# Optimization experiments

Hardware: AMD Instinct MI355X
Metric: run time of the kernel (lower is better)

## Reference

```python
import jax, jax.numpy as jnp
import numpy as np

H, C, PQ, PV = 12, 16, 4, 8  # heads, scalar head dim, query points, value points
EPS = 1e-8


def setup_inputs() -> dict:
    key = jax.random.key(0)
    ks = jax.random.split(key, 16)
    B, N, S, Z = 2, 512, 384, 128
    def w(k, fan_in, shape):
        return jax.random.normal(k, shape, jnp.float32) / np.sqrt(fan_in)
    return {
        's': jax.random.normal(ks[0], (B, N, S), jnp.float32),
        'z': jax.random.normal(ks[1], (B, N, N, Z), jnp.float32),
        'R': jax.random.normal(ks[2], (B, N, 3, 3), jnp.float32),
        't': jax.random.normal(ks[3], (B, N, 3), jnp.float32),
        'Wq': w(ks[4], S, (S, H * C)),
        'Wk': w(ks[5], S, (S, H * C)),
        'Wv': w(ks[6], S, (S, H * C)),
        'Wqp': w(ks[7], S, (S, H * PQ * 3)),
        'Wkp': w(ks[8], S, (S, H * PQ * 3)),
        'Wvp': w(ks[9], S, (S, H * PV * 3)),
        'Wb': w(ks[10], Z, (Z, H)),
        'head_weights': jax.random.normal(ks[11], (H,), jnp.float32) * 0.1,
        'Wout': w(ks[12], H * (C + 4 * PV + Z), (H * (C + 4 * PV + Z), S)),
    }


def reference(s, z, R, t, Wq, Wk, Wv, Wqp, Wkp, Wvp, Wb, head_weights, Wout):
    B, N, _ = s.shape
    Zc = z.shape[-1]
    # scalar q/k/v: [B,N,H,C]
    q = (s @ Wq).reshape(B, N, H, C)
    k = (s @ Wk).reshape(B, N, H, C)
    v = (s @ Wv).reshape(B, N, H, C)
    # point q/k/v in local frames, then map to global: x_g = R x + t
    def to_global(Wp, P):
        p = (s @ Wp).reshape(B, N, H, P, 3)
        return jnp.einsum('bnxy,bnhpy->bnhpx', R, p) + t[:, :, None, None, :]
    qp = to_global(Wqp, PQ)   # [B,N,H,PQ,3]
    kp = to_global(Wkp, PQ)
    vp = to_global(Wvp, PV)   # [B,N,H,PV,3]
    # pair bias [B,H,N,N]
    b = jnp.einsum('bijz,zh->bhij', z, Wb)
    # scalar attention logits
    scal = jnp.einsum('bihc,bjhc->bhij', q, k) / np.sqrt(C)
    # squared point distances via expansion (avoid [B,N,N,H,PQ,3] tensor)
    qq = jnp.sum(qp * qp, axis=(-1, -2))                    # [B,N,H]
    kk = jnp.sum(kp * kp, axis=(-1, -2))                    # [B,N,H]
    qk = jnp.einsum('bihpx,bjhpx->bhij', qp, kp)
    dist2 = qq.transpose(0, 2, 1)[:, :, :, None] + kk.transpose(0, 2, 1)[:, :, None, :] - 2.0 * qk
    gamma = jax.nn.softplus(head_weights)                   # [H]
    wC = np.sqrt(2.0 / (9.0 * PQ))
    wL = np.sqrt(1.0 / 3.0)
    logits = wL * (scal + b) - (wL * wC / 2.0) * gamma[None, :, None, None] * dist2
    a = jax.nn.softmax(logits, axis=-1)                     # [B,H,N,N]
    # scalar output
    o = jnp.einsum('bhij,bjhc->bihc', a, v).reshape(B, N, H * C)
    # point output: aggregate in global frame, then back to local: R^T (x - t)
    opt_g = jnp.einsum('bhij,bjhpx->bihpx', a, vp)
    d = opt_g - t[:, :, None, None, :]
    opt = jnp.einsum('bnyx,bnhpy->bnhpx', R, d)             # R^T d
    opt_norm = jnp.sqrt(jnp.sum(opt * opt, axis=-1) + EPS)  # [B,N,H,PV]
    # pair output
    opair = jnp.einsum('bhij,bijz->bihz', a, z).reshape(B, N, H * Zc)
    cat = jnp.concatenate([o, opt.reshape(B, N, H * PV * 3),
                           opt_norm.reshape(B, N, H * PV), opair], axis=-1)
    return cat @ Wout
```

## Files before the change

### kernel.cpp

```cpp
#include <hip/hip_runtime.h>
#include <math.h>

#define BB 2
#define NN 512
#define SDIM 384
#define ZDIM 128
#define HH 12
#define CDIM 16
#define PQ 4
#define PV 8
#define BN (BB*NN)
#define CATD 2112

#define WL  0.57735026918962576f
#define LAM 0.06804138174397717f

#define OFF_Q    0
#define OFF_QP   196608
#define OFF_QQ   344064
#define OFF_KT4  356352
#define OFF_KPT4 552960
#define OFF_KKT  700416
#define OFF_V    712704
#define OFF_VP   909312
#define OFF_CAT  7495680

__device__ __forceinline__ float dot4(float4 a, float4 b) {
    return a.x*b.x + a.y*b.y + a.z*b.z + a.w*b.w;
}
__device__ __forceinline__ void fma4(float4& a, float s, float4 b) {
    a.x += s*b.x; a.y += s*b.y; a.z += s*b.z; a.w += s*b.w;
}
__device__ __forceinline__ void add4(float4& a, float4 b) {
    a.x += b.x; a.y += b.y; a.z += b.z; a.w += b.w;
}
__device__ __forceinline__ void mul4(float4& a, float s) {
    a.x *= s; a.y *= s; a.z *= s; a.w *= s;
}

__global__ __launch_bounds__(256) void k_proj(
    const float* __restrict__ s, const float* __restrict__ Rg, const float* __restrict__ tg,
    const float* __restrict__ Wq, const float* __restrict__ Wk, const float* __restrict__ Wv,
    const float* __restrict__ Wqp, const float* __restrict__ Wkp, const float* __restrict__ Wvp,
    float* __restrict__ ws)
{
    __shared__ float4 pL4[2][144];
    __shared__ float  sqL[2][96];
    __shared__ float  Rt[2][12];
    const int t = threadIdx.x;
    const int n0 = blockIdx.x * 2;
    const int b  = n0 >> 9;
    const int nloc = n0 & 511;

    if (t < 24) {
        int rr = t / 12, c = t % 12;
        Rt[rr][c] = (c < 9) ? Rg[(n0+rr)*9 + c] : tg[(n0+rr)*3 + (c-9)];
    }
    const float* s0 = s + (size_t)n0*SDIM;
    const float* s1 = s0 + SDIM;
    __syncthreads();

    float4* Q4g  = (float4*)(ws + OFF_Q);
    float4* V4g  = (float4*)(ws + OFF_V);
    float4* KT4g = (float4*)(ws + OFF_KT4);

    for (int it = 0; it < 2; ++it) {
        int g = t + it*256;
        if (g >= 288) break;
        const float4* W4; int wc4, ld4, dst;
        if (g < 48)       { W4 = (const float4*)Wq;  wc4 = g;     ld4 = 48; dst = 0; }
        else if (g < 96)  { W4 = (const float4*)Wk;  wc4 = g-48;  ld4 = 48; dst = 1; }
        else if (g < 144) { W4 = (const float4*)Wv;  wc4 = g-96;  ld4 = 48; dst = 2; }
        else if (g < 180) { W4 = (const float4*)Wqp; wc4 = g-144; ld4 = 36; dst = 3; }
        else if (g < 216) { W4 = (const float4*)Wkp; wc4 = g-180; ld4 = 36; dst = 4; }
        else              { W4 = (const float4*)Wvp; wc4 = g-216; ld4 = 72; dst = 5; }
        float4 acc0 = {0,0,0,0}, acc1 = {0,0,0,0};
        #pragma unroll 4
        for (int r = 0; r < SDIM; ++r) {
            float4 wv = W4[r*ld4 + wc4];
            float f0 = s0[r], f1 = s1[r];
            fma4(acc0, f0, wv);
            fma4(acc1, f1, wv);
        }
        if (dst == 0) {
            Q4g[(size_t)n0*48 + wc4] = acc0;
            Q4g[(size_t)(n0+1)*48 + wc4] = acc1;
        } else if (dst == 1) {
            size_t base = ((size_t)(b*48 + wc4))*512 + nloc;
            KT4g[base] = acc0; KT4g[base+1] = acc1;
        } else if (dst == 2) {
            V4g[(size_t)n0*48 + wc4] = acc0;
            V4g[(size_t)(n0+1)*48 + wc4] = acc1;
        } else if (dst == 3) {
            pL4[0][wc4] = acc0; pL4[1][wc4] = acc1;
        } else if (dst == 4) {
            pL4[0][36+wc4] = acc0; pL4[1][36+wc4] = acc1;
        } else {
            pL4[0][72+wc4] = acc0; pL4[1][72+wc4] = acc1;
        }
    }
    __syncthreads();

    for (int task = t; task < 384; task += 256) {
        int rr = task / 192, pt = task % 192;
        const float* pl = (const float*)pL4[rr];
        int off = (pt < 48) ? pt*3 : (pt < 96 ? 144 + (pt-48)*3 : 288 + (pt-96)*3);
        float p0 = pl[off], p1 = pl[off+1], p2 = pl[off+2];
        const float* R = Rt[rr];
        float g0 = R[0]*p0 + R[1]*p1 + R[2]*p2 + R[9];
        float g1 = R[3]*p0 + R[4]*p1 + R[5]*p2 + R[10];
        float g2 = R[6]*p0 + R[7]*p1 + R[8]*p2 + R[11];
        int bn = n0 + rr, n = bn & 511;
        if (pt < 48) {
            int o = pt*3;
            float* d = ws + OFF_QP + (size_t)bn*144 + o;
            d[0] = g0; d[1] = g1; d[2] = g2;
            sqL[rr][pt] = g0*g0 + g1*g1 + g2*g2;
        } else if (pt < 96) {
            int pc = (pt-48)*3;
            float gg[3] = {g0,g1,g2};
            #pragma unroll
            for (int x = 0; x < 3; ++x) {
                int pcx = pc + x;
                ws[OFF_KPT4 + (((size_t)(b*36 + (pcx>>2)))*512 + n)*4 + (pcx&3)] = gg[x];
            }
            sqL[rr][pt] = g0*g0 + g1*g1 + g2*g2;
        } else {
            int o = (pt-96)*3;
            float* d = ws + OFF_VP + (size_t)bn*288 + o;
            d[0] = g0; d[1] = g1; d[2] = g2;
        }
    }
    __syncthreads();

    if (t < 48) {
        int rr = t / 24, u = t % 24;
        int bn = n0 + rr, n = bn & 511;
        if (u < 12) {
            float sm = sqL[rr][u*4] + sqL[rr][u*4+1] + sqL[rr][u*4+2] + sqL[rr][u*4+3];
            ws[OFF_QQ + (size_t)bn*12 + u] = sm;
        } else {
            int h = u - 12;
            float sm = sqL[rr][48+h*4] + sqL[rr][48+h*4+1] + sqL[rr][48+h*4+2] + sqL[rr][48+h*4+3];
            ws[OFF_KKT + ((size_t)(b*12 + h))*512 + n] = sm;
        }
    }
}

__global__ __launch_bounds__(512, 2) void k_attn(
    const float* __restrict__ z, const float* __restrict__ Rg, const float* __restrict__ tg,
    const float* __restrict__ hw, const float* __restrict__ Wb, float* __restrict__ ws)
{
    __shared__ __align__(16) float aL[8448];
    __shared__ float4 optgS4[72];
    __shared__ float RiL[9], tiL[3], sInv[12];

    const int t = threadIdx.x;
    const int d = blockIdx.x;
    const int xcd = d & 7, slot = d >> 3;
    const int bi = (xcd < 4) ? (xcd*128 + slot) : (512 + (xcd-4)*128 + slot);
    const int b = bi >> 9;

    if (t < 9)             RiL[t]   = Rg[bi*9 + t];
    if (t >= 9 && t < 12)  tiL[t-9] = tg[bi*3 + (t-9)];

    float gam[HH];
    #pragma unroll
    for (int h = 0; h < HH; ++h) {
        float x = hw[h];
        gam[h] = (x > 20.f) ? x : log1pf(__expf(x));
    }

    {
        const int j = t;
        float pb[HH];
        #pragma unroll
        for (int h = 0; h < HH; ++h) pb[h] = 0.f;
        const float4* zrow4 = (const float4*)z + ((size_t)bi*512 + j)*32;
        #pragma unroll 4
        for (int c4 = 0; c4 < 32; ++c4) {
            const float4 zq = zrow4[c4];
            const float* wb = Wb + c4*48;
            #pragma unroll
            for (int e = 0; e < 4; ++e) {
                const float zv = ((const float*)&zq)[e];
                const float* w = wb + e*12;
                #pragma unroll
                for (int h = 0; h < HH; ++h) pb[h] += zv * w[h];
            }
        }
        const float4* Q4u  = (const float4*)(ws + OFF_Q  + (size_t)bi*192);
        const float4* QP4u = (const float4*)(ws + OFF_QP + (size_t)bi*144);
        const float*  QQu  = ws + OFF_QQ + (size_t)bi*12;
        const float4* KT4  = (const float4*)(ws + OFF_KT4)  + (size_t)b*48*512;
        const float4* KPT4 = (const float4*)(ws + OFF_KPT4) + (size_t)b*36*512;
        const float*  KKT  = ws + OFF_KKT  + (size_t)b*12*512;
        for (int h = 0; h < HH; ++h) {
            float scal = 0.f, qk = 0.f;
            #pragma unroll
            for (int cg = 0; cg < 4; ++cg)
                scal += dot4(Q4u[h*4+cg], KT4[(h*4+cg)*512 + j]);
            #pragma unroll
            for (int pg = 0; pg < 3; ++pg)
                qk += dot4(QP4u[h*3+pg], KPT4[(h*3+pg)*512 + j]);
            float dist2 = QQu[h] + KKT[h*512 + j] - 2.f*qk;
            aL[h*516 + j] = WL*(scal*0.25f + pb[h]) - LAM*gam[h]*dist2;
        }
    }
    __syncthreads();

    {
        const int w = t >> 6, lane = t & 63;
        for (int h = w; h < HH; h += 8) {
            float* row = aL + h*516;
            float m = -1e30f;
            #pragma unroll
            for (int k = 0; k < 8; ++k) m = fmaxf(m, row[lane + 64*k]);
            #pragma unroll
            for (int off = 32; off > 0; off >>= 1) m = fmaxf(m, __shfl_xor(m, off));
            float ssum = 0.f;
            #pragma unroll
            for (int k = 0; k < 8; ++k) {
                float e = __expf(row[lane + 64*k] - m);
                row[lane + 64*k] = e;
                ssum += e;
            }
            #pragma unroll
            for (int off = 32; off > 0; off >>= 1) ssum += __shfl_xor(ssum, off);
            if (lane == 0) sInv[h] = 1.f / ssum;
        }
    }
    __syncthreads();

    float4 acc0={0,0,0,0}, acc1={0,0,0,0}, acc2={0,0,0,0};
    float4 acc3={0,0,0,0}, acc4={0,0,0,0}, acc5={0,0,0,0};

    if (t < 192) {
        const int seg0 = t / 64;
        const int r = t & 63;
        const int q = r >> 5, zc4 = r & 31;
        const int j0 = seg0*176;
        const int ngrp = (seg0 == 2) ? 20 : 22;
        const float4* Zp = (const float4*)z + (size_t)bi*512*32 + zc4;
        const float* aA0 = aL + (q   )*516;
        const float* aA1 = aL + (q+4 )*516;
        const float* aA2 = aL + (q+8 )*516;
        const float* aB0 = aL + (q+2 )*516;
        const float* aB1 = aL + (q+6 )*516;
        const float* aB2 = aL + (q+10)*516;

#define FMA8_6(ZB, JT) do { \
    float4 vA0 = *(const float4*)(aA0 + (JT)); float4 wA0 = *(const float4*)(aA0 + (JT) + 4); \
    float4 vA1 = *(const float4*)(aA1 + (JT)); float4 wA1 = *(const float4*)(aA1 + (JT) + 4); \
    float4 vA2 = *(const float4*)(aA2 + (JT)); float4 wA2 = *(const float4*)(aA2 + (JT) + 4); \
    float4 vB0 = *(const float4*)(aB0 + (JT)); float4 wB0 = *(const float4*)(aB0 + (JT) + 4); \
    float4 vB1 = *(const float4*)(aB1 + (JT)); float4 wB1 = *(const float4*)(aB1 + (JT) + 4); \
    float4 vB2 = *(const float4*)(aB2 + (JT)); float4 wB2 = *(const float4*)(aB2 + (JT) + 4); \
    fma4(acc0, vA0.x, ZB[0]); fma4(acc1, vA1.x, ZB[0]); fma4(acc2, vA2.x, ZB[0]); \
    fma4(acc3, vB0.x, ZB[0]); fma4(acc4, vB1.x, ZB[0]); fma4(acc5, vB2.x, ZB[0]); \
    fma4(acc0, vA0.y, ZB[1]); fma4(acc1, vA1.y, ZB[1]); fma4(acc2, vA2.y, ZB[1]); \
    fma4(acc3, vB0.y, ZB[1]); fma4(acc4, vB1.y, ZB[1]); fma4(acc5, vB2.y, ZB[1]); \
    fma4(acc0, vA0.z, ZB[2]); fma4(acc1, vA1.z, ZB[2]); fma4(acc2, vA2.z, ZB[2]); \
    fma4(acc3, vB0.z, ZB[2]); fma4(acc4, vB1.z, ZB[2]); fma4(acc5, vB2.z, ZB[2]); \
    fma4(acc0, vA0.w, ZB[3]); fma4(acc1, vA1.w, ZB[3]); fma4(acc2, vA2.w, ZB[3]); \
    fma4(acc3, vB0.w, ZB[3]); fma4(acc4, vB1.w, ZB[3]); fma4(acc5, vB2.w, ZB[3]); \
    fma4(acc0, wA0.x, ZB[4]); fma4(acc1, wA1.x, ZB[4]); fma4(acc2, wA2.x, ZB[4]); \
    fma4(acc3, wB0.x, ZB[4]); fma4(acc4, wB1.x, ZB[4]); fma4(acc5, wB2.x, ZB[4]); \
    fma4(acc0, wA0.y, ZB[5]); fma4(acc1, wA1.y, ZB[5]); fma4(acc2, wA2.y, ZB[5]); \
    fma4(acc3, wB0.y, ZB[5]); fma4(acc4, wB1.y, ZB[5]); fma4(acc5, wB2.y, ZB[5]); \
    fma4(acc0, wA0.z, ZB[6]); fma4(acc1, wA1.z, ZB[6]); fma4(acc2, wA2.z, ZB[6]); \
    fma4(acc3, wB0.z, ZB[6]); fma4(acc4, wB1.z, ZB[6]); fma4(acc5, wB2.z, ZB[6]); \
    fma4(acc0, wA0.w, ZB[7]); fma4(acc1, wA1.w, ZB[7]); fma4(acc2, wA2.w, ZB[7]); \
    fma4(acc3, wB0.w, ZB[7]); fma4(acc4, wB1.w, ZB[7]); fma4(acc5, wB2.w, ZB[7]); \
} while (0)

        float4 zA[8], zB[8];
        #pragma unroll
        for (int e = 0; e < 8; ++e) zA[e] = Zp[(size_t)(j0+e)*32];
        for (int p = 0; p < ngrp; p += 2) {
            const int jt = j0 + p*8;
            #pragma unroll
            for (int e = 0; e < 8; ++e) zB[e] = Zp[(size_t)(jt+8+e)*32];
            FMA8_6(zA, jt);
            if (p + 2 < ngrp) {
                #pragma unroll
                for (int e = 0; e < 8; ++e) zA[e] = Zp[(size_t)(jt+16+e)*32];
            }
            FMA8_6(zB, jt + 8);
        }
#undef FMA8_6
    } else {
        const int v = t - 192;
        const int seg8 = v / 40;
        const int w = v % 40;
        const int j0 = seg8*64, j1 = j0 + 64;
        const float4* P; int S, D, O, hg;
        if (w < 16) {
            hg = w >> 2; S = 48; D = 16; O = hg*4 + (w & 3);
            P = (const float4*)(ws + OFF_V) + (size_t)b*512*48;
        } else {
            const int v2 = w - 16;
            hg = v2 / 6; S = 72; D = 24; O = hg*6 + v2 % 6;
            P = (const float4*)(ws + OFF_VP) + (size_t)b*512*72;
        }
        const float* a0p = aL + hg*516;
        const float* a1p = aL + (hg+4)*516;
        const float* a2p = aL + (hg+8)*516;
        #pragma unroll 2
        for (int jt = j0; jt < j1; jt += 4) {
            float4 av0 = *(const float4*)(a0p + jt);
            float4 av1 = *(const float4*)(a1p + jt);
            float4 av2 = *(const float4*)(a2p + jt);
            #pragma unroll
            for (int e = 0; e < 4; ++e) {
                const size_t base = (size_t)(jt+e)*S + O;
                fma4(acc0, ((const float*)&av0)[e], P[base]);
                fma4(acc1, ((const float*)&av1)[e], P[base + D]);
                fma4(acc2, ((const float*)&av2)[e], P[base + 2*D]);
            }
        }
    }
    __syncthreads();
    float4* sc4 = (float4*)aL;
    if (t < 192) {
        const int si = t*6;
        sc4[si]   = acc0; sc4[si+1] = acc1; sc4[si+2] = acc2;
        sc4[si+3] = acc3; sc4[si+4] = acc4; sc4[si+5] = acc5;
    } else {
        const int si = 1152 + (t-192)*3;
        sc4[si] = acc0; sc4[si+1] = acc1; sc4[si+2] = acc2;
    }
    __syncthreads();

    if (t < 168) {
        float4 r0 = {0,0,0,0}, r1 = {0,0,0,0}, r2 = {0,0,0,0};
        float4* cat4 = (float4*)(ws + OFF_CAT);
        const size_t cb = (size_t)bi * 528;
        if (t < 128) {
            const int hg = t >> 5, zc4 = t & 31;
            const int q = hg & 1, half = hg >> 1;
            #pragma unroll
            for (int ss = 0; ss < 3; ++ss) {
                const int si = (ss*64 + q*32 + zc4)*6 + half*3;
                add4(r0, sc4[si]); add4(r1, sc4[si+1]); add4(r2, sc4[si+2]);
            }
            mul4(r0, sInv[hg]); mul4(r1, sInv[hg+4]); mul4(r2, sInv[hg+8]);
            cat4[cb + 144 + (hg  )*32 + zc4] = r0;
            cat4[cb + 144 + (hg+4)*32 + zc4] = r1;
            cat4[cb + 144 + (hg+8)*32 + zc4] = r2;
        } else {
            const int w = t - 128;
            #pragma unroll
            for (int ss = 0; ss < 8; ++ss) {
                const int si = 1152 + (ss*40 + w)*3;
                add4(r0, sc4[si]); add4(r1, sc4[si+1]); add4(r2, sc4[si+2]);
            }
            if (w < 16) {
                const int hg = w >> 2, c4 = w & 3;
                mul4(r0, sInv[hg]); mul4(r1, sInv[hg+4]); mul4(r2, sInv[hg+8]);
                cat4[cb + (hg  )*4 + c4] = r0;
                cat4[cb + (hg+4)*4 + c4] = r1;
                cat4[cb + (hg+8)*4 + c4] = r2;
            } else {
                const int v2 = w - 16;
                const int hg = v2 / 6, po = v2 % 6;
                mul4(r0, sInv[hg]); mul4(r1, sInv[hg+4]); mul4(r2, sInv[hg+8]);
                optgS4[(hg  )*6 + po] = r0;
                optgS4[(hg+4)*6 + po] = r1;
                optgS4[(hg+8)*6 + po] = r2;
            }
        }
    }
    __syncthreads();

    if (t < 96) {
        const float* og = (const float*)optgS4;
        int h = t >> 3, p = t & 7;
        int o = h*24 + p*3;
        float d0 = og[o]   - tiL[0];
        float d1 = og[o+1] - tiL[1];
        float d2 = og[o+2] - tiL[2];
        float ox = RiL[0]*d0 + RiL[3]*d1 + RiL[6]*d2;
        float oy = RiL[1]*d0 + RiL[4]*d1 + RiL[7]*d2;
        float oz = RiL[2]*d0 + RiL[5]*d1 + RiL[8]*d2;
        float* cat = ws + OFF_CAT + (size_t)bi*CATD;
        cat[192 + o]     = ox;
        cat[192 + o + 1] = oy;
        cat[192 + o + 2] = oz;
        cat[480 + h*8 + p] = sqrtf(ox*ox + oy*oy + oz*oz + 1e-8f);
    }
}

__global__ __launch_bounds__(384) void k_out(
    const float* __restrict__ Wout, const float* __restrict__ ws, float* __restrict__ out)
{
    __shared__ __align__(16) float catS[4*CATD];
    const int t = threadIdx.x;
    const int row0 = blockIdx.x * 4;
    {
        const float4* src = (const float4*)(ws + OFF_CAT + (size_t)row0*CATD);
        float4* dst = (float4*)catS;
        #pragma unroll
        for (int i = t; i < 4*528; i += 384) dst[i] = src[i];
    }
    __syncthreads();
    const float* c0 = catS;
    const float* c1 = catS + CATD;
    const float* c2 = catS + 2*CATD;
    const float* c3 = catS + 3*CATD;
    float a0 = 0.f, a1 = 0.f, a2 = 0.f, a3 = 0.f;
    #pragma unroll 8
    for (int r = 0; r < CATD; ++r) {
        float w = Wout[(size_t)r*384 + t];
        a0 += c0[r]*w; a1 += c1[r]*w; a2 += c2[r]*w; a3 += c3[r]*w;
    }
    out[(size_t)(row0+0)*384 + t] = a0;
    out[(size_t)(row0+1)*384 + t] = a1;
    out[(size_t)(row0+2)*384 + t] = a2;
    out[(size_t)(row0+3)*384 + t] = a3;
}

extern "C" void kernel_launch(void* const* d_in, const int* in_sizes, int n_in,
                              void* d_out, int out_size, void* d_ws, size_t ws_size,
                              hipStream_t stream)
{
    const float* s    = (const float*)d_in[0];
    const float* z    = (const float*)d_in[1];
    const float* R    = (const float*)d_in[2];
    const float* tt   = (const float*)d_in[3];
    const float* Wq   = (const float*)d_in[4];
    const float* Wk   = (const float*)d_in[5];
    const float* Wv   = (const float*)d_in[6];
    const float* Wqp  = (const float*)d_in[7];
    const float* Wkp  = (const float*)d_in[8];
    const float* Wvp  = (const float*)d_in[9];
    const float* Wb   = (const float*)d_in[10];
    const float* hw   = (const float*)d_in[11];
    const float* Wout = (const float*)d_in[12];
    float* ws  = (float*)d_ws;
    float* out = (float*)d_out;

    hipLaunchKernelGGL(k_proj, dim3(BN/2), dim3(256), 0, stream,
                       s, R, tt, Wq, Wk, Wv, Wqp, Wkp, Wvp, ws);
    hipLaunchKernelGGL(k_attn, dim3(BN),   dim3(512), 0, stream, z, R, tt, hw, Wb, ws);
    hipLaunchKernelGGL(k_out,  dim3(BN/4), dim3(384), 0, stream, Wout, ws, out);
}
```

Before: 725.7 us.

## Stage z tiles through padded LDS for coalesced pair-bias computation

The pair-bias projection previously had each thread read its own z row of 128 floats, so a wavefront's accesses were strided by 512 bytes. It now loads 64-row chunks of z into a padded shared buffer with coalesced loads. Eight threads each reduce 16 channels and combine partials with shuffles, writing the bias into the logits buffer. This adds LDS use (about 33KB extra) and extra syncs, which may lower occupancy under launch bounds of 2 blocks. The softmax-to-scratch reuse now targets the new buffer, which removes one barrier.

```diff
diff --git a/kernel.cpp b/kernel.cpp
--- a/kernel.cpp
+++ b/kernel.cpp
@@ -151,7 +151,8 @@
     const float* __restrict__ z, const float* __restrict__ Rg, const float* __restrict__ tg,
     const float* __restrict__ hw, const float* __restrict__ Wb, float* __restrict__ ws)
 {
-    __shared__ __align__(16) float aL[8448];
+    __shared__ __align__(16) float4 zs4[2112];
+    __shared__ __align__(16) float aL[HH*516];
     __shared__ float4 optgS4[72];
     __shared__ float RiL[9], tiL[3], sInv[12];
 
@@ -164,31 +165,51 @@
     if (t < 9)             RiL[t]   = Rg[bi*9 + t];
     if (t >= 9 && t < 12)  tiL[t-9] = tg[bi*3 + (t-9)];
 
-    float gam[HH];
-    #pragma unroll
-    for (int h = 0; h < HH; ++h) {
-        float x = hw[h];
-        gam[h] = (x > 20.f) ? x : log1pf(__expf(x));
-    }
+    {
+        const float4* zg4 = (const float4*)z + (size_t)bi*512*32;
+        const int jj = t >> 3;
+        const int oc = t & 7;
+        for (int ch = 0; ch < 8; ++ch) {
+            __syncthreads();
+            #pragma unroll
+            for (int k2 = 0; k2 < 4; ++k2) {
+                const int i = t + 512*k2;
+                zs4[(i>>5)*33 + (i&31)] = zg4[ch*2048 + i];
+            }
+            __syncthreads();
+            float pb[HH];
+            #pragma unroll
+            for (int h = 0; h < HH; ++h) pb[h] = 0.f;
+            #pragma unroll
+            for (int c = 0; c < 4; ++c) {
+                const float4 zq = zs4[jj*33 + oc*4 + c];
+                const float* wb = Wb + (oc*16 + c*4)*12;
+                #pragma unroll
+                for (int e = 0; e < 4; ++e) {
+                    const float zv = ((const float*)&zq)[e];
+                    const float* w = wb + e*12;
+                    #pragma unroll
+                    for (int h = 0; h < HH; ++h) pb[h] += zv * w[h];
+                }
+            }
+            #pragma unroll
+            for (int h = 0; h < HH; ++h) {
+                pb[h] += __shfl_xor(pb[h], 1);
+                pb[h] += __shfl_xor(pb[h], 2);
+                pb[h] += __shfl_xor(pb[h], 4);
+            }
+            if (oc < 4) {
+                const int j = ch*64 + jj;
+                aL[(oc  )*516 + j] = pb[oc];
+                aL[(oc+4)*516 + j] = pb[oc+4];
+                aL[(oc+8)*516 + j] = pb[oc+8];
+            }
+        }
+    }
+    __syncthreads();
 
     {
         const int j = t;
-        float pb[HH];
-        #pragma unroll
-        for (int h = 0; h < HH; ++h) pb[h] = 0.f;
-        const float4* zrow4 = (const float4*)z + ((size_t)bi*512 + j)*32;
-        #pragma unroll 4
-        for (int c4 = 0; c4 < 32; ++c4) {
-            const float4 zq = zrow4[c4];
-            const float* wb = Wb + c4*48;
-            #pragma unroll
-            for (int e = 0; e < 4; ++e) {
-                const float zv = ((const float*)&zq)[e];
-                const float* w = wb + e*12;
-                #pragma unroll
-                for (int h = 0; h < HH; ++h) pb[h] += zv * w[h];
-            }
-        }
         const float4* Q4u  = (const float4*)(ws + OFF_Q  + (size_t)bi*192);
         const float4* QP4u = (const float4*)(ws + OFF_QP + (size_t)bi*144);
         const float*  QQu  = ws + OFF_QQ + (size_t)bi*12;
@@ -196,6 +217,8 @@
         const float4* KPT4 = (const float4*)(ws + OFF_KPT4) + (size_t)b*36*512;
         const float*  KKT  = ws + OFF_KKT  + (size_t)b*12*512;
         for (int h = 0; h < HH; ++h) {
+            const float x = hw[h];
+            const float gam = (x > 20.f) ? x : log1pf(__expf(x));
             float scal = 0.f, qk = 0.f;
             #pragma unroll
             for (int cg = 0; cg < 4; ++cg)
@@ -203,8 +226,8 @@
             #pragma unroll
             for (int pg = 0; pg < 3; ++pg)
                 qk += dot4(QP4u[h*3+pg], KPT4[(h*3+pg)*512 + j]);
-            float dist2 = QQu[h] + KKT[h*512 + j] - 2.f*qk;
-            aL[h*516 + j] = WL*(scal*0.25f + pb[h]) - LAM*gam[h]*dist2;
+            const float dist2 = QQu[h] + KKT[h*512 + j] - 2.f*qk;
+            aL[h*516 + j] = WL*(scal*0.25f + aL[h*516 + j]) - LAM*gam*dist2;
         }
     }
     __syncthreads();
@@ -320,8 +343,7 @@
             }
         }
     }
-    __syncthreads();
-    float4* sc4 = (float4*)aL;
+    float4* sc4 = zs4;
     if (t < 192) {
         const int si = t*6;
         sc4[si]   = acc0; sc4[si+1] = acc1; sc4[si+2] = acc2;
```

New measurement: 792.3 us. +9.2%, slower.

## Repartition z aggregation so each thread covers all 12 heads over a j-segment

Applied to the files above, without the earlier changes.

The pair-output stage (a·z) is reassigned so that 128 threads each handle all 12 heads for one 4-float z column chunk over a 128-row j segment. Previously 192 threads each covered 6 heads over roughly 176 rows. Each z element is now loaded from global memory once per block rather than twice, which cuts z traffic, the dominant memory stream. The cost is 12 float4 accumulators per thread, which raises register pressure, and fewer threads issuing z loads. Shared memory for the reduction grows and 64 threads go idle in this phase.

```diff
diff --git a/kernel.cpp b/kernel.cpp
--- a/kernel.cpp
+++ b/kernel.cpp
@@ -151,7 +151,7 @@
     const float* __restrict__ z, const float* __restrict__ Rg, const float* __restrict__ tg,
     const float* __restrict__ hw, const float* __restrict__ Wb, float* __restrict__ ws)
 {
-    __shared__ __align__(16) float aL[8448];
+    __shared__ __align__(16) float aL[9984];
     __shared__ float4 optgS4[72];
     __shared__ float RiL[9], tiL[3], sInv[12];
 
@@ -232,65 +232,48 @@
     }
     __syncthreads();
 
+    float4 accT[HH];
+    #pragma unroll
+    for (int h = 0; h < HH; ++h) accT[h] = make_float4(0.f, 0.f, 0.f, 0.f);
     float4 acc0={0,0,0,0}, acc1={0,0,0,0}, acc2={0,0,0,0};
-    float4 acc3={0,0,0,0}, acc4={0,0,0,0}, acc5={0,0,0,0};
-
-    if (t < 192) {
-        const int seg0 = t / 64;
-        const int r = t & 63;
-        const int q = r >> 5, zc4 = r & 31;
-        const int j0 = seg0*176;
-        const int ngrp = (seg0 == 2) ? 20 : 22;
+
+    if (t < 128) {
+        const int seg0 = t >> 5;
+        const int zc4 = t & 31;
+        const int j0 = seg0*128;
         const float4* Zp = (const float4*)z + (size_t)bi*512*32 + zc4;
-        const float* aA0 = aL + (q   )*516;
-        const float* aA1 = aL + (q+4 )*516;
-        const float* aA2 = aL + (q+8 )*516;
-        const float* aB0 = aL + (q+2 )*516;
-        const float* aB1 = aL + (q+6 )*516;
-        const float* aB2 = aL + (q+10)*516;
-
-#define FMA8_6(ZB, JT) do { \
-    float4 vA0 = *(const float4*)(aA0 + (JT)); float4 wA0 = *(const float4*)(aA0 + (JT) + 4); \
-    float4 vA1 = *(const float4*)(aA1 + (JT)); float4 wA1 = *(const float4*)(aA1 + (JT) + 4); \
-    float4 vA2 = *(const float4*)(aA2 + (JT)); float4 wA2 = *(const float4*)(aA2 + (JT) + 4); \
-    float4 vB0 = *(const float4*)(aB0 + (JT)); float4 wB0 = *(const float4*)(aB0 + (JT) + 4); \
-    float4 vB1 = *(const float4*)(aB1 + (JT)); float4 wB1 = *(const float4*)(aB1 + (JT) + 4); \
-    float4 vB2 = *(const float4*)(aB2 + (JT)); float4 wB2 = *(const float4*)(aB2 + (JT) + 4); \
-    fma4(acc0, vA0.x, ZB[0]); fma4(acc1, vA1.x, ZB[0]); fma4(acc2, vA2.x, ZB[0]); \
-    fma4(acc3, vB0.x, ZB[0]); fma4(acc4, vB1.x, ZB[0]); fma4(acc5, vB2.x, ZB[0]); \
-    fma4(acc0, vA0.y, ZB[1]); fma4(acc1, vA1.y, ZB[1]); fma4(acc2, vA2.y, ZB[1]); \
-    fma4(acc3, vB0.y, ZB[1]); fma4(acc4, vB1.y, ZB[1]); fma4(acc5, vB2.y, ZB[1]); \
-    fma4(acc0, vA0.z, ZB[2]); fma4(acc1, vA1.z, ZB[2]); fma4(acc2, vA2.z, ZB[2]); \
-    fma4(acc3, vB0.z, ZB[2]); fma4(acc4, vB1.z, ZB[2]); fma4(acc5, vB2.z, ZB[2]); \
-    fma4(acc0, vA0.w, ZB[3]); fma4(acc1, vA1.w, ZB[3]); fma4(acc2, vA2.w, ZB[3]); \
-    fma4(acc3, vB0.w, ZB[3]); fma4(acc4, vB1.w, ZB[3]); fma4(acc5, vB2.w, ZB[3]); \
-    fma4(acc0, wA0.x, ZB[4]); fma4(acc1, wA1.x, ZB[4]); fma4(acc2, wA2.x, ZB[4]); \
-    fma4(acc3, wB0.x, ZB[4]); fma4(acc4, wB1.x, ZB[4]); fma4(acc5, wB2.x, ZB[4]); \
-    fma4(acc0, wA0.y, ZB[5]); fma4(acc1, wA1.y, ZB[5]); fma4(acc2, wA2.y, ZB[5]); \
-    fma4(acc3, wB0.y, ZB[5]); fma4(acc4, wB1.y, ZB[5]); fma4(acc5, wB2.y, ZB[5]); \
-    fma4(acc0, wA0.z, ZB[6]); fma4(acc1, wA1.z, ZB[6]); fma4(acc2, wA2.z, ZB[6]); \
-    fma4(acc3, wB0.z, ZB[6]); fma4(acc4, wB1.z, ZB[6]); fma4(acc5, wB2.z, ZB[6]); \
-    fma4(acc0, wA0.w, ZB[7]); fma4(acc1, wA1.w, ZB[7]); fma4(acc2, wA2.w, ZB[7]); \
-    fma4(acc3, wB0.w, ZB[7]); fma4(acc4, wB1.w, ZB[7]); fma4(acc5, wB2.w, ZB[7]); \
+        const float* arow[HH];
+        #pragma unroll
+        for (int h = 0; h < HH; ++h) arow[h] = aL + h*516;
+
+#define FMA4_12(ZB, JT) do { \
+    _Pragma("unroll") \
+    for (int h = 0; h < HH; ++h) { \
+        const float4 av = *(const float4*)(arow[h] + (JT)); \
+        fma4(accT[h], av.x, ZB[0]); \
+        fma4(accT[h], av.y, ZB[1]); \
+        fma4(accT[h], av.z, ZB[2]); \
+        fma4(accT[h], av.w, ZB[3]); \
+    } \
 } while (0)
 
-        float4 zA[8], zB[8];
+        float4 zA[4], zB[4];
         #pragma unroll
-        for (int e = 0; e < 8; ++e) zA[e] = Zp[(size_t)(j0+e)*32];
-        for (int p = 0; p < ngrp; p += 2) {
-            const int jt = j0 + p*8;
-            #pragma unroll
-            for (int e = 0; e < 8; ++e) zB[e] = Zp[(size_t)(jt+8+e)*32];
-            FMA8_6(zA, jt);
-            if (p + 2 < ngrp) {
+        for (int e = 0; e < 4; ++e) zA[e] = Zp[(size_t)(j0+e)*32];
+        for (int p = 0; p < 32; p += 2) {
+            const int jt = j0 + p*4;
+            #pragma unroll
+            for (int e = 0; e < 4; ++e) zB[e] = Zp[(size_t)(jt+4+e)*32];
+            FMA4_12(zA, jt);
+            if (p + 2 < 32) {
                 #pragma unroll
-                for (int e = 0; e < 8; ++e) zA[e] = Zp[(size_t)(jt+16+e)*32];
-            }
-            FMA8_6(zB, jt + 8);
-        }
-#undef FMA8_6
-    } else {
-        const int v = t - 192;
+                for (int e = 0; e < 4; ++e) zA[e] = Zp[(size_t)(jt+8+e)*32];
+            }
+            FMA4_12(zB, jt + 4);
+        }
+#undef FMA4_12
+    } else if (t < 448) {
+        const int v = t - 128;
         const int seg8 = v / 40;
         const int w = v % 40;
         const int j0 = seg8*64, j1 = j0 + 64;
@@ -322,12 +305,12 @@
     }
     __syncthreads();
     float4* sc4 = (float4*)aL;
-    if (t < 192) {
-        const int si = t*6;
-        sc4[si]   = acc0; sc4[si+1] = acc1; sc4[si+2] = acc2;
-        sc4[si+3] = acc3; sc4[si+4] = acc4; sc4[si+5] = acc5;
-    } else {
-        const int si = 1152 + (t-192)*3;
+    if (t < 128) {
+        const int si = t*12;
+        #pragma unroll
+        for (int h = 0; h < HH; ++h) sc4[si + h] = accT[h];
+    } else if (t < 448) {
+        const int si = 1536 + (t-128)*3;
         sc4[si] = acc0; sc4[si+1] = acc1; sc4[si+2] = acc2;
     }
     __syncthreads();
@@ -338,11 +321,12 @@
         const size_t cb = (size_t)bi * 528;
         if (t < 128) {
             const int hg = t >> 5, zc4 = t & 31;
-            const int q = hg & 1, half = hg >> 1;
-            #pragma unroll
-            for (int ss = 0; ss < 3; ++ss) {
-                const int si = (ss*64 + q*32 + zc4)*6 + half*3;
-                add4(r0, sc4[si]); add4(r1, sc4[si+1]); add4(r2, sc4[si+2]);
+            #pragma unroll
+            for (int ss = 0; ss < 4; ++ss) {
+                const int si = (ss*32 + zc4)*12;
+                add4(r0, sc4[si + hg]);
+                add4(r1, sc4[si + hg + 4]);
+                add4(r2, sc4[si + hg + 8]);
             }
             mul4(r0, sInv[hg]); mul4(r1, sInv[hg+4]); mul4(r2, sInv[hg+8]);
             cat4[cb + 144 + (hg  )*32 + zc4] = r0;
@@ -352,7 +336,7 @@
             const int w = t - 128;
             #pragma unroll
             for (int ss = 0; ss < 8; ++ss) {
-                const int si = 1152 + (ss*40 + w)*3;
+                const int si = 1536 + (ss*40 + w)*3;
                 add4(r0, sc4[si]); add4(r1, sc4[si+1]); add4(r2, sc4[si+2]);
             }
             if (w < 16) {
```

Measured after the change: 731.7 us. No clear change (+0.8%).
